# Kernel optimization log

Hardware: AMD Instinct MI355X
Metric: run time of the kernel (lower is better)

## Reference

```python
import jax, jax.numpy as jnp
import numpy as np

N_NODES = 150001   # users + 1 (social graph)
DIM = 64
N_EDGES = 3_000_000
N_LAYERS = 3       # layer_sg


def _masked_segment_softmax(w, mask, dst, n):
    # scatter_softmax over retained edges, grouped by destination node.
    neg = jnp.finfo(w.dtype).min
    logits = jnp.where(mask, w, neg)
    m = jax.ops.segment_max(logits, dst, num_segments=n)          # [n]
    m_safe = jnp.where(m > neg * 0.5, m, 0.0)                      # guard empty groups
    e = jnp.where(mask, jnp.exp(w - m_safe[dst]), 0.0)             # [E]
    s = jax.ops.segment_sum(e, dst, num_segments=n)                # [n]
    return e / jnp.maximum(s[dst], 1e-16)


def setup_inputs() -> dict:
    key = jax.random.key(0)
    k1, k2, k3, k4 = jax.random.split(key, 4)
    emb = jax.random.normal(k1, (N_NODES, DIM), dtype=jnp.float32) * 0.05
    edge_attr = jax.random.uniform(k2, (N_EDGES,), dtype=jnp.float32)
    edge_index = jax.random.randint(k3, (2, N_EDGES), 0, N_NODES, dtype=jnp.int64)
    # one dropout mask per propagation layer (rand <= edge_attr semantics,
    # precomputed so the reference is deterministic)
    edge_mask = jax.random.uniform(k4, (N_LAYERS, N_EDGES)) <= edge_attr[None, :]
    return {"emb": emb, "edge_attr": edge_attr,
            "edge_index": edge_index, "edge_mask": edge_mask}


def reference(emb, edge_attr, edge_index, edge_mask):
    # HDSR.compute(..., dtype='soc', perturbed=True):
    # per layer: edge dropout -> scatter_softmax edge weights -> LGConv
    # (gcn_norm, no self loops, weighted propagation) -> stack & mean layers.
    src = edge_index[0]
    dst = edge_index[1]
    n = emb.shape[0]
    x = emb
    acc = emb
    for l in range(edge_mask.shape[0]):
        mask = edge_mask[l]
        ew = _masked_segment_softmax(edge_attr, mask, dst, n)      # [E]
        # gcn_norm (add_self_loops=False): deg over col, D^-1/2 A D^-1/2
        deg = jax.ops.segment_sum(ew, dst, num_segments=n)         # [n]
        dis = jnp.where(deg > 0,
                        jax.lax.rsqrt(jnp.maximum(deg, 1e-16)), 0.0)
        norm = dis[src] * ew * dis[dst]                            # [E]
        # propagate: out[dst] += norm * x[src]
        x = jax.ops.segment_sum(norm[:, None] * x[src], dst, num_segments=n)
        acc = acc + x
    return acc / (edge_mask.shape[0] + 1)
```

## Files before the change

kernel.cpp:

```cpp
#include <hip/hip_runtime.h>
#include <hip/hip_fp16.h>


constexpr int N     = 150001;
constexpr int E     = 3000000;
constexpr int NB    = (N + 255) / 256;
constexpr int PB    = (N + 3) / 4;
constexpr int SLOTS = 64;

using u16 = unsigned short;

__device__ __forceinline__ float h2f(u16 u) { __half h; *(u16*)&h = u; return __half2float(h); }
__device__ __forceinline__ u16  f2h(float f) { __half h = __float2half_rn(f); return *(u16*)&h; }

__global__ void detect_kernel(const unsigned int* __restrict__ ei_w,
                              const unsigned int* __restrict__ mask_w,
                              int* __restrict__ flags) {
    __shared__ int hi_nonzero, not01;
    if (threadIdx.x == 0) { hi_nonzero = 0; not01 = 0; }
    __syncthreads();
    for (int i = threadIdx.x; i < 4096; i += blockDim.x) {
        if (ei_w[2 * i + 1] != 0u) hi_nonzero = 1;
        if (mask_w[i] > 1u)        not01 = 1;
    }
    __syncthreads();
    if (threadIdx.x == 0) {
        flags[0] = (hi_nonzero == 0) ? 1 : 0;
        flags[1] = not01;
    }
}

__device__ __forceinline__ int load_node(const void* ei, int idx, int f64) {
    return f64 ? (int)((const long long*)ei)[idx] : ((const int*)ei)[idx];
}

__global__ void prep_kernel(const void* __restrict__ ei, const void* __restrict__ maskp,
                            const float* __restrict__ attr, const int* __restrict__ flags,
                            int* __restrict__ cnt, int* __restrict__ csr4) {
    const int f64 = flags[0], fu8 = flags[1];
    const unsigned char* m8 = (const unsigned char*)maskp;
    const int* m32 = (const int*)maskp;
    for (int e = blockIdx.x * blockDim.x + threadIdx.x; e < E; e += gridDim.x * blockDim.x) {
        const int s_ = load_node(ei, e, f64);
        const int d  = load_node(ei, E + e, f64);
        unsigned int mb;
        if (fu8) mb = (m8[e]  ? 1u : 0u) | (m8[E + e]  ? 2u : 0u) | (m8[2 * E + e]  ? 4u : 0u);
        else     mb = (m32[e] ? 1u : 0u) | (m32[E + e] ? 2u : 0u) | (m32[2 * E + e] ? 4u : 0u);
        const int rank = atomicAdd(&cnt[d], 1);
        const int aq = (int)(attr[e] * 2047.0f + 0.5f);
        if (rank < SLOTS)
            csr4[(d << 6) + rank] = s_ | (int)(mb << 18) | (aq << 21);
    }
}

__global__ __launch_bounds__(256) void sums_kernel(const int* __restrict__ cnt,
                                                   const int* __restrict__ csr4,
                                                   float* __restrict__ invs,
                                                   unsigned char* __restrict__ flagb) {
    const int n = blockIdx.x * blockDim.x + threadIdx.x;
    if (n >= N) return;
    const int beg = n << 6;
    const int end = beg + min(cnt[n], SLOTS);
    float s0 = 0.f, s1 = 0.f, s2 = 0.f;
    for (int p = beg; p < end; ++p) {
        const int v = csr4[p];
        const float ex = __expf((float)((unsigned)v >> 21) * (1.0f / 2047.0f));
        if (v & (1 << 18)) s0 += ex;
        if (v & (1 << 19)) s1 += ex;
        if (v & (1 << 20)) s2 += ex;
    }
    invs[n]         = s0 > 0.f ? 1.f / s0 : 0.f;
    invs[N + n]     = s1 > 0.f ? 1.f / s1 : 0.f;
    invs[2 * N + n] = s2 > 0.f ? 1.f / s2 : 0.f;
    flagb[n] = (unsigned char)((s0 > 0.f ? 1 : 0) | (s1 > 0.f ? 2 : 0) | (s2 > 0.f ? 4 : 0));
}

__global__ void conv_kernel(const float* __restrict__ emb, u16* __restrict__ x0h) {
    const int M = (N * 64) / 4;
    for (int i = blockIdx.x * blockDim.x + threadIdx.x; i < M; i += gridDim.x * blockDim.x) {
        const float4 f = reinterpret_cast<const float4*>(emb)[i];
        ushort4 u;
        u.x = f2h(f.x); u.y = f2h(f.y); u.z = f2h(f.z); u.w = f2h(f.w);
        reinterpret_cast<ushort4*>(x0h)[i] = u;
    }
}

template <int L>
__global__ __launch_bounds__(256) void prop_kernel(const int* __restrict__ cnt,
                                                   const int* __restrict__ csr4,
                                                   const float* __restrict__ invs_l,
                                                   const unsigned char* __restrict__ flagb,
                                                   const u16* __restrict__ xin,
                                                   u16* __restrict__ xout) {
    const int wid = (int)((blockIdx.x * blockDim.x + threadIdx.x) >> 6);
    if (wid >= N) return;
    const int lane = threadIdx.x & 63;
    const int g  = lane >> 3;
    const int sl = lane & 7;
    float acc[8] = {0.f, 0.f, 0.f, 0.f, 0.f, 0.f, 0.f, 0.f};
    const float inv = invs_l[wid];
    if (inv != 0.f) {
        const int beg = wid << 6;
        const int end = beg + min(cnt[wid], SLOTS);
        const int mbit = 1 << (18 + L);
        const unsigned char fbit = (unsigned char)(1 << L);
        for (int p = beg + g; p < end; p += 8) {
            const int v = csr4[p];
            if (v & mbit) {
                const int sidx = v & 0x3FFFF;
                if (flagb[sidx] & fbit) {
                    const float a = (float)((unsigned)v >> 21) * (1.0f / 2047.0f);
                    const float c = __expf(a) * inv;
                    const uint4 q = *reinterpret_cast<const uint4*>(
                        xin + ((size_t)sidx << 6) + (sl << 3));
                    const __half2* hp = reinterpret_cast<const __half2*>(&q);
#pragma unroll
                    for (int j = 0; j < 4; ++j) {
                        const float2 f = __half22float2(hp[j]);
                        acc[2 * j]     = fmaf(c, f.x, acc[2 * j]);
                        acc[2 * j + 1] = fmaf(c, f.y, acc[2 * j + 1]);
                    }
                }
            }
        }
    }
#pragma unroll
    for (int m = 8; m < 64; m <<= 1) {
#pragma unroll
        for (int j = 0; j < 8; ++j) acc[j] += __shfl_xor(acc[j], m, 64);
    }
    if (lane < 8) {
        uint4 w;
        w.x = (unsigned)f2h(acc[0]) | ((unsigned)f2h(acc[1]) << 16);
        w.y = (unsigned)f2h(acc[2]) | ((unsigned)f2h(acc[3]) << 16);
        w.z = (unsigned)f2h(acc[4]) | ((unsigned)f2h(acc[5]) << 16);
        w.w = (unsigned)f2h(acc[6]) | ((unsigned)f2h(acc[7]) << 16);
        *reinterpret_cast<uint4*>(xout + ((size_t)wid << 6) + (sl << 3)) = w;
    }
}

__global__ __launch_bounds__(256) void prop2fin_kernel(const int* __restrict__ cnt,
                                                       const int* __restrict__ csr4,
                                                       const float* __restrict__ invs_l,
                                                       const unsigned char* __restrict__ flagb,
                                                       const u16* __restrict__ x1h,
                                                       const u16* __restrict__ x2h,
                                                       const float* __restrict__ emb,
                                                       float* __restrict__ out) {
    const int wid = (int)((blockIdx.x * blockDim.x + threadIdx.x) >> 6);
    if (wid >= N) return;
    const int lane = threadIdx.x & 63;
    const int g  = lane >> 3;
    const int sl = lane & 7;
    float acc[8] = {0.f, 0.f, 0.f, 0.f, 0.f, 0.f, 0.f, 0.f};
    const float inv = invs_l[wid];
    if (inv != 0.f) {
        const int beg = wid << 6;
        const int end = beg + min(cnt[wid], SLOTS);
        const int mbit = 1 << 20;
        for (int p = beg + g; p < end; p += 8) {
            const int v = csr4[p];
            if (v & mbit) {
                const int sidx = v & 0x3FFFF;
                if (flagb[sidx] & 4) {
                    const float a = (float)((unsigned)v >> 21) * (1.0f / 2047.0f);
                    const float c = __expf(a) * inv;
                    const uint4 q = *reinterpret_cast<const uint4*>(
                        x2h + ((size_t)sidx << 6) + (sl << 3));
                    const __half2* hp = reinterpret_cast<const __half2*>(&q);
#pragma unroll
                    for (int j = 0; j < 4; ++j) {
                        const float2 f = __half22float2(hp[j]);
                        acc[2 * j]     = fmaf(c, f.x, acc[2 * j]);
                        acc[2 * j + 1] = fmaf(c, f.y, acc[2 * j + 1]);
                    }
                }
            }
        }
    }
#pragma unroll
    for (int m = 8; m < 64; m <<= 1) {
#pragma unroll
        for (int j = 0; j < 8; ++j) acc[j] += __shfl_xor(acc[j], m, 64);
    }
    if (lane < 8) {
        const size_t base = ((size_t)wid << 6) + (sl << 3);
        const uint4 q1 = *reinterpret_cast<const uint4*>(x1h + base);
        const uint4 q2 = *reinterpret_cast<const uint4*>(x2h + base);
        const __half2* h1 = reinterpret_cast<const __half2*>(&q1);
        const __half2* h2 = reinterpret_cast<const __half2*>(&q2);
        const float4 e0 = *reinterpret_cast<const float4*>(emb + base);
        const float4 e1 = *reinterpret_cast<const float4*>(emb + base + 4);
        float o[8];
#pragma unroll
        for (int j = 0; j < 4; ++j) {
            const float2 f1 = __half22float2(h1[j]);
            const float2 f2 = __half22float2(h2[j]);
            o[2 * j]     = f1.x + f2.x + acc[2 * j];
            o[2 * j + 1] = f1.y + f2.y + acc[2 * j + 1];
        }
        float4 w0, w1;
        w0.x = 0.25f * (e0.x + o[0]); w0.y = 0.25f * (e0.y + o[1]);
        w0.z = 0.25f * (e0.z + o[2]); w0.w = 0.25f * (e0.w + o[3]);
        w1.x = 0.25f * (e1.x + o[4]); w1.y = 0.25f * (e1.y + o[5]);
        w1.z = 0.25f * (e1.z + o[6]); w1.w = 0.25f * (e1.w + o[7]);
        *reinterpret_cast<float4*>(out + base)     = w0;
        *reinterpret_cast<float4*>(out + base + 4) = w1;
    }
}

extern "C" void kernel_launch(void* const* d_in, const int* in_sizes, int n_in,
                              void* d_out, int out_size, void* d_ws, size_t ws_size,
                              hipStream_t stream) {
    const float* emb   = (const float*)d_in[0];
    const float* attr  = (const float*)d_in[1];
    const void*  ei    = d_in[2];
    const void*  maskp = d_in[3];
    float* out = (float*)d_out;

    char* w = (char*)d_ws;
    auto alloc = [&](size_t b) -> char* {
        char* p = w;
        w += (b + 255) & ~(size_t)255;
        return p;
    };
    int* flags           = (int*)alloc(2 * sizeof(int));
    int* cnt             = (int*)alloc((size_t)N * 4);
    float* invs          = (float*)alloc((size_t)3 * N * 4);
    unsigned char* flagb = (unsigned char*)alloc((size_t)N);
    int* csr4            = (int*)alloc((size_t)N * SLOTS * 4);
    u16* x0h             = (u16*)alloc((size_t)N * 64 * 2);
    u16* x1h             = (u16*)alloc((size_t)N * 64 * 2);
    u16* x2h             = (u16*)alloc((size_t)N * 64 * 2);
    if ((size_t)(w - (char*)d_ws) > ws_size) return;

    hipMemsetAsync(cnt, 0, (size_t)N * 4, stream);
    detect_kernel<<<1, 256, 0, stream>>>((const unsigned int*)ei, (const unsigned int*)maskp, flags);
    prep_kernel<<<2048, 256, 0, stream>>>(ei, maskp, attr, flags, cnt, csr4);
    sums_kernel<<<NB, 256, 0, stream>>>(cnt, csr4, invs, flagb);
    conv_kernel<<<2048, 256, 0, stream>>>(emb, x0h);
    prop_kernel<0><<<PB, 256, 0, stream>>>(cnt, csr4, invs,     flagb, x0h, x1h);
    prop_kernel<1><<<PB, 256, 0, stream>>>(cnt, csr4, invs + N, flagb, x1h, x2h);
    prop2fin_kernel<<<PB, 256, 0, stream>>>(cnt, csr4, invs + 2 * N, flagb, x1h, x2h, emb, out);
}
```

Before: 595.4 us.

## Build destination CSR via bucketed partition instead of global atomics

Replaces the single scatter pass, which did a global atomicAdd per edge on per-node counters, and the separate softmax-sum kernel with a multi-pass bucket partition. Edges are histogrammed into 1024-node buckets per block, scanned, and partitioned into a temporary buffer. A per-bucket kernel then fills the slot CSR and accumulates the softmax denominators with shared-memory atomics. The aim is to turn random global atomics and scattered writes into localized shared-memory work. The cost is five extra launches plus an extra write and read pass over the edges, with the partition buffer aliased onto the unused x1/x2 buffers.

New measurement: 532.5 us. 1.12x faster.

```diff
diff --git a/kernel.cpp b/kernel.cpp
--- a/kernel.cpp
+++ b/kernel.cpp
@@ -4,9 +4,11 @@
 
 constexpr int N     = 150001;
 constexpr int E     = 3000000;
-constexpr int NB    = (N + 255) / 256;
 constexpr int PB    = (N + 3) / 4;
 constexpr int SLOTS = 64;
+constexpr int NBKT  = 147;
+constexpr int PBLK  = 512;
+constexpr int PCH   = (E + PBLK - 1) / PBLK;
 
 using u16 = unsigned short;
 
@@ -34,45 +36,125 @@
     return f64 ? (int)((const long long*)ei)[idx] : ((const int*)ei)[idx];
 }
 
-__global__ void prep_kernel(const void* __restrict__ ei, const void* __restrict__ maskp,
-                            const float* __restrict__ attr, const int* __restrict__ flags,
-                            int* __restrict__ cnt, int* __restrict__ csr4) {
+__global__ __launch_bounds__(256) void p1_hist(const void* __restrict__ ei,
+                                               const int* __restrict__ flags,
+                                               int* __restrict__ blk_hist) {
+    __shared__ int h[NBKT];
+    for (int i = threadIdx.x; i < NBKT; i += 256) h[i] = 0;
+    __syncthreads();
+    const int f64 = flags[0];
+    const int b = blockIdx.x;
+    const int e0 = b * PCH, e1 = min(E, e0 + PCH);
+    for (int e = e0 + (int)threadIdx.x; e < e1; e += 256)
+        atomicAdd(&h[load_node(ei, E + e, f64) >> 10], 1);
+    __syncthreads();
+    for (int i = threadIdx.x; i < NBKT; i += 256) blk_hist[i * PBLK + b] = h[i];
+}
+
+__global__ __launch_bounds__(512) void p2a_rowscan(const int* __restrict__ blk_hist,
+                                                   int* __restrict__ rowscan,
+                                                   int* __restrict__ totals) {
+    __shared__ int sd[512];
+    const int k = blockIdx.x, t = threadIdx.x;
+    const int v = blk_hist[k * PBLK + t];
+    sd[t] = v;
+    __syncthreads();
+    for (int off = 1; off < 512; off <<= 1) {
+        int tmp = 0;
+        if (t >= off) tmp = sd[t - off];
+        __syncthreads();
+        if (t >= off) sd[t] += tmp;
+        __syncthreads();
+    }
+    rowscan[k * PBLK + t] = sd[t] - v;
+    if (t == 511) totals[k] = sd[511];
+}
+
+__global__ void p2b_base(const int* __restrict__ totals, int* __restrict__ base) {
+    __shared__ int sd[256];
+    const int t = threadIdx.x;
+    const int v = (t < NBKT) ? totals[t] : 0;
+    sd[t] = v;
+    __syncthreads();
+    for (int off = 1; off < 256; off <<= 1) {
+        int tmp = 0;
+        if (t >= off) tmp = sd[t - off];
+        __syncthreads();
+        if (t >= off) sd[t] += tmp;
+        __syncthreads();
+    }
+    if (t < NBKT) base[t] = sd[t] - v;
+    if (t == 0) base[NBKT] = E;
+}
+
+__global__ __launch_bounds__(256) void p3_part(const void* __restrict__ ei,
+                                               const void* __restrict__ maskp,
+                                               const float* __restrict__ attr,
+                                               const int* __restrict__ flags,
+                                               const int* __restrict__ base,
+                                               const int* __restrict__ rowscan,
+                                               int2* __restrict__ part) {
+    __shared__ int off_l[NBKT], cur[NBKT];
+    const int b = blockIdx.x;
+    for (int i = threadIdx.x; i < NBKT; i += 256) {
+        off_l[i] = base[i] + rowscan[i * PBLK + b];
+        cur[i] = 0;
+    }
+    __syncthreads();
     const int f64 = flags[0], fu8 = flags[1];
     const unsigned char* m8 = (const unsigned char*)maskp;
     const int* m32 = (const int*)maskp;
-    for (int e = blockIdx.x * blockDim.x + threadIdx.x; e < E; e += gridDim.x * blockDim.x) {
+    const int e0 = b * PCH, e1 = min(E, e0 + PCH);
+    for (int e = e0 + (int)threadIdx.x; e < e1; e += 256) {
         const int s_ = load_node(ei, e, f64);
         const int d  = load_node(ei, E + e, f64);
         unsigned int mb;
         if (fu8) mb = (m8[e]  ? 1u : 0u) | (m8[E + e]  ? 2u : 0u) | (m8[2 * E + e]  ? 4u : 0u);
         else     mb = (m32[e] ? 1u : 0u) | (m32[E + e] ? 2u : 0u) | (m32[2 * E + e] ? 4u : 0u);
-        const int rank = atomicAdd(&cnt[d], 1);
         const int aq = (int)(attr[e] * 2047.0f + 0.5f);
+        const int k = d >> 10;
+        const int r = atomicAdd(&cur[k], 1);
+        part[off_l[k] + r] = make_int2(d | (int)(mb << 18), s_ | (aq << 18));
+    }
+}
+
+__global__ __launch_bounds__(1024) void p4_build(const int2* __restrict__ part,
+                                                 const int* __restrict__ base,
+                                                 int* __restrict__ csr4,
+                                                 int* __restrict__ cnt,
+                                                 float* __restrict__ invs,
+                                                 unsigned char* __restrict__ flagb) {
+    __shared__ int lcnt[1024];
+    __shared__ float ls0[1024], ls1[1024], ls2[1024];
+    const int k = blockIdx.x, t = threadIdx.x;
+    lcnt[t] = 0; ls0[t] = 0.f; ls1[t] = 0.f; ls2[t] = 0.f;
+    __syncthreads();
+    const int p0 = base[k], p1 = base[k + 1];
+    for (int p = p0 + t; p < p1; p += 1024) {
+        const int2 v = part[p];
+        const int d   = v.x & 0x3FFFF;
+        const int mb  = (v.x >> 18) & 7;
+        const int src = v.y & 0x3FFFF;
+        const int aq  = (v.y >> 18) & 0x7FF;
+        const int dl  = d & 1023;
+        const int rank = atomicAdd(&lcnt[dl], 1);
         if (rank < SLOTS)
-            csr4[(d << 6) + rank] = s_ | (int)(mb << 18) | (aq << 21);
-    }
-}
-
-__global__ __launch_bounds__(256) void sums_kernel(const int* __restrict__ cnt,
-                                                   const int* __restrict__ csr4,
-                                                   float* __restrict__ invs,
-                                                   unsigned char* __restrict__ flagb) {
-    const int n = blockIdx.x * blockDim.x + threadIdx.x;
-    if (n >= N) return;
-    const int beg = n << 6;
-    const int end = beg + min(cnt[n], SLOTS);
-    float s0 = 0.f, s1 = 0.f, s2 = 0.f;
-    for (int p = beg; p < end; ++p) {
-        const int v = csr4[p];
-        const float ex = __expf((float)((unsigned)v >> 21) * (1.0f / 2047.0f));
-        if (v & (1 << 18)) s0 += ex;
-        if (v & (1 << 19)) s1 += ex;
-        if (v & (1 << 20)) s2 += ex;
-    }
-    invs[n]         = s0 > 0.f ? 1.f / s0 : 0.f;
-    invs[N + n]     = s1 > 0.f ? 1.f / s1 : 0.f;
-    invs[2 * N + n] = s2 > 0.f ? 1.f / s2 : 0.f;
-    flagb[n] = (unsigned char)((s0 > 0.f ? 1 : 0) | (s1 > 0.f ? 2 : 0) | (s2 > 0.f ? 4 : 0));
+            csr4[((size_t)d << 6) + rank] = src | (mb << 18) | (aq << 21);
+        const float ex = __expf((float)aq * (1.0f / 2047.0f));
+        if (mb & 1) atomicAdd(&ls0[dl], ex);
+        if (mb & 2) atomicAdd(&ls1[dl], ex);
+        if (mb & 4) atomicAdd(&ls2[dl], ex);
+    }
+    __syncthreads();
+    const int n = (k << 10) + t;
+    if (n < N) {
+        cnt[n] = lcnt[t];
+        const float s0 = ls0[t], s1 = ls1[t], s2 = ls2[t];
+        invs[n]         = s0 > 0.f ? 1.f / s0 : 0.f;
+        invs[N + n]     = s1 > 0.f ? 1.f / s1 : 0.f;
+        invs[2 * N + n] = s2 > 0.f ? 1.f / s2 : 0.f;
+        flagb[n] = (unsigned char)((s0 > 0.f ? 1 : 0) | (s1 > 0.f ? 2 : 0) | (s2 > 0.f ? 4 : 0));
+    }
 }
 
 __global__ void conv_kernel(const float* __restrict__ emb, u16* __restrict__ x0h) {
@@ -184,13 +266,13 @@
         for (int j = 0; j < 8; ++j) acc[j] += __shfl_xor(acc[j], m, 64);
     }
     if (lane < 8) {
-        const size_t base = ((size_t)wid << 6) + (sl << 3);
-        const uint4 q1 = *reinterpret_cast<const uint4*>(x1h + base);
-        const uint4 q2 = *reinterpret_cast<const uint4*>(x2h + base);
+        const size_t base_ = ((size_t)wid << 6) + (sl << 3);
+        const uint4 q1 = *reinterpret_cast<const uint4*>(x1h + base_);
+        const uint4 q2 = *reinterpret_cast<const uint4*>(x2h + base_);
         const __half2* h1 = reinterpret_cast<const __half2*>(&q1);
         const __half2* h2 = reinterpret_cast<const __half2*>(&q2);
-        const float4 e0 = *reinterpret_cast<const float4*>(emb + base);
-        const float4 e1 = *reinterpret_cast<const float4*>(emb + base + 4);
+        const float4 e0 = *reinterpret_cast<const float4*>(emb + base_);
+        const float4 e1 = *reinterpret_cast<const float4*>(emb + base_ + 4);
         float o[8];
 #pragma unroll
         for (int j = 0; j < 4; ++j) {
@@ -204,8 +286,8 @@
         w0.z = 0.25f * (e0.z + o[2]); w0.w = 0.25f * (e0.w + o[3]);
         w1.x = 0.25f * (e1.x + o[4]); w1.y = 0.25f * (e1.y + o[5]);
         w1.z = 0.25f * (e1.z + o[6]); w1.w = 0.25f * (e1.w + o[7]);
-        *reinterpret_cast<float4*>(out + base)     = w0;
-        *reinterpret_cast<float4*>(out + base + 4) = w1;
+        *reinterpret_cast<float4*>(out + base_)     = w0;
+        *reinterpret_cast<float4*>(out + base_ + 4) = w1;
     }
 }
 
@@ -228,16 +310,25 @@
     int* cnt             = (int*)alloc((size_t)N * 4);
     float* invs          = (float*)alloc((size_t)3 * N * 4);
     unsigned char* flagb = (unsigned char*)alloc((size_t)N);
+    int* blk_hist        = (int*)alloc((size_t)NBKT * PBLK * 4);
+    int* rowscan         = (int*)alloc((size_t)NBKT * PBLK * 4);
+    int* totals          = (int*)alloc((size_t)NBKT * 4);
+    int* basep           = (int*)alloc((size_t)(NBKT + 1) * 4);
     int* csr4            = (int*)alloc((size_t)N * SLOTS * 4);
-    u16* x0h             = (u16*)alloc((size_t)N * 64 * 2);
-    u16* x1h             = (u16*)alloc((size_t)N * 64 * 2);
-    u16* x2h             = (u16*)alloc((size_t)N * 64 * 2);
+    u16* xall            = (u16*)alloc((size_t)3 * N * 64 * 2);
     if ((size_t)(w - (char*)d_ws) > ws_size) return;
 
-    hipMemsetAsync(cnt, 0, (size_t)N * 4, stream);
+    u16* x0h = xall;
+    u16* x1h = xall + (size_t)N * 64;
+    u16* x2h = xall + (size_t)2 * N * 64;
+    int2* part = (int2*)x1h;
+
     detect_kernel<<<1, 256, 0, stream>>>((const unsigned int*)ei, (const unsigned int*)maskp, flags);
-    prep_kernel<<<2048, 256, 0, stream>>>(ei, maskp, attr, flags, cnt, csr4);
-    sums_kernel<<<NB, 256, 0, stream>>>(cnt, csr4, invs, flagb);
+    p1_hist<<<PBLK, 256, 0, stream>>>(ei, flags, blk_hist);
+    p2a_rowscan<<<NBKT, 512, 0, stream>>>(blk_hist, rowscan, totals);
+    p2b_base<<<1, 256, 0, stream>>>(totals, basep);
+    p3_part<<<PBLK, 256, 0, stream>>>(ei, maskp, attr, flags, basep, rowscan, part);
+    p4_build<<<NBKT, 1024, 0, stream>>>(part, basep, csr4, cnt, invs, flagb);
     conv_kernel<<<2048, 256, 0, stream>>>(emb, x0h);
     prop_kernel<0><<<PB, 256, 0, stream>>>(cnt, csr4, invs,     flagb, x0h, x1h);
     prop_kernel<1><<<PB, 256, 0, stream>>>(cnt, csr4, invs + N, flagb, x1h, x2h);
```
